# Performance work log

Hardware: AMD Instinct MI355X
Metric: run time of the kernel (lower is better)

The kernel has to match this reference:

```python
import jax, jax.numpy as jnp
import numpy as np

B, MAX_ATOM, F = 512, 256, 256
L_IN, L_OUT = 2, 1


def setup_inputs() -> dict:
    key = jax.random.key(0)
    ks = jax.random.split(key, 8)
    return {
        "node_features": jax.random.normal(ks[0], (B, MAX_ATOM, F), dtype=jnp.float32),
        "inblock_acts": jax.random.normal(ks[1], (L_IN, B, MAX_ATOM, F), dtype=jnp.float32),
        "block_outputs": jax.random.normal(ks[2], (L_OUT, B, MAX_ATOM, F), dtype=jnp.float32),
        "mol_slice": jax.random.randint(ks[3], (B,), 1, MAX_ATOM + 1, dtype=jnp.int32),
        "W_in": jax.random.normal(ks[4], (L_IN, F, F), dtype=jnp.float32) * (1.0 / np.sqrt(F)),
        "W_out": jax.random.normal(ks[5], (L_OUT, F, F), dtype=jnp.float32) * (1.0 / np.sqrt(F)),
        "beta1": jnp.ones((1,), dtype=jnp.float32),
        "beta2": jnp.ones((1,), dtype=jnp.float32),
    }


def reference(node_features, inblock_acts, block_outputs, mol_slice, W_in, W_out, beta1, beta2):
    # Row mask replaces per-graph dynamic slice + zero pad: masked rows stay 0
    # through the row-wise matmuls and through ReLU(0)=0.
    max_atom = node_features.shape[1]
    mask = (jnp.arange(max_atom)[None, :] < mol_slice[:, None]).astype(node_features.dtype)[:, :, None]  # [B,M,1]
    # multi-residual matmul-accumulate over inblock layers and preceding blocks
    x = node_features
    x = x + beta1[0] * jnp.einsum('lbmf,lfo->bmo', inblock_acts, W_in)
    x = x + beta2[0] * jnp.einsum('pbmf,pfo->bmo', block_outputs, W_out)
    return jax.nn.relu(x * mask)  # [B, max_atom, F]
```

## Files before the change

### kernel.cpp

```cpp
#include <hip/hip_runtime.h>
#include <hip/hip_bf16.h>


#define BATCH  512
#define MAXA   256
#define FDIM   256
#define KTOT   768
#define ROWS   131072
#define TILE_M 128
#define BK     64
#define KPAD   72

typedef __attribute__((ext_vector_type(8))) short  short8;
typedef __attribute__((ext_vector_type(4))) float  fx4;

__device__ __forceinline__ unsigned short f2bf(float x) {
  unsigned int u = __builtin_bit_cast(unsigned int, x);
  u += 0x7fffu + ((u >> 16) & 1u);
  return (unsigned short)(u >> 16);
}

__device__ __forceinline__ short8 cvt8(fx4 a, fx4 b) {
  short8 r;
  r[0] = (short)f2bf(a[0]); r[1] = (short)f2bf(a[1]);
  r[2] = (short)f2bf(a[2]); r[3] = (short)f2bf(a[3]);
  r[4] = (short)f2bf(b[0]); r[5] = (short)f2bf(b[1]);
  r[6] = (short)f2bf(b[2]); r[7] = (short)f2bf(b[3]);
  return r;
}

__global__ void prep_weights(const float* __restrict__ Win,
                             const float* __restrict__ Wout,
                             const float* __restrict__ b1,
                             const float* __restrict__ b2,
                             unsigned short* __restrict__ Wt) {
  int id = blockIdx.x * 256 + threadIdx.x;
  int n = id / KTOT;
  int k = id - n * KTOT;
  float beta, w;
  if (k < 512) { beta = b1[0]; w = Win[k * FDIM + n]; }
  else         { beta = b2[0]; w = Wout[(k - 512) * FDIM + n]; }
  Wt[id] = f2bf(beta * w);
}

__launch_bounds__(512, 4)
__global__ void fused_main(const float* __restrict__ node,
                           const float* __restrict__ acts,
                           const float* __restrict__ bouts,
                           const int*   __restrict__ mol_slice,
                           const unsigned short* __restrict__ Wt,
                           float* __restrict__ out) {
  const int tile  = blockIdx.x;
  const int bmol  = tile >> 1;
  const int m0    = (tile & 1) << 7;
  const int slice = mol_slice[bmol];
  const int t     = threadIdx.x;
  const long rowBase = (long)tile * TILE_M;

  if (slice <= m0) {
    fx4 z = {0.f, 0.f, 0.f, 0.f};
    fx4* o4 = (fx4*)(out + rowBase * FDIM);
#pragma unroll
    for (int i = 0; i < 16; ++i) o4[i * 512 + t] = z;
    return;
  }

  __shared__ unsigned short Xs[TILE_M][KPAD];
  __shared__ unsigned short Ws[FDIM][KPAD];

  const int lane = t & 63;
  const int wv   = t >> 6;
  const int wm   = (wv >> 2) << 6;
  const int wn   = (wv & 3) << 6;

  fx4 acc[4][4];
#pragma unroll
  for (int i = 0; i < 4; ++i)
#pragma unroll
    for (int j = 0; j < 4; ++j) acc[i][j] = (fx4){0.f, 0.f, 0.f, 0.f};

  const int xrow = t >> 2;
  const int xc   = (t & 3) << 4;
  const bool xact = (m0 + xrow) < slice;
  const int wrow = t >> 1;
  const int wc   = (t & 1) << 5;

  for (int kk = 0; kk < KTOT; kk += BK) {
    const float* src = (kk < 256) ? acts : ((kk < 512) ? (acts + 33554432) : bouts);
    const int klocal = kk & 255;

    if (xact) {
      const fx4* g = (const fx4*)(src + (rowBase + xrow) * FDIM + klocal + xc);
      fx4 v0 = g[0], v1 = g[1], v2 = g[2], v3 = g[3];
      *(short8*)&Xs[xrow][xc]     = cvt8(v0, v1);
      *(short8*)&Xs[xrow][xc + 8] = cvt8(v2, v3);
    }
    {
      const int4* g = (const int4*)(Wt + (size_t)wrow * KTOT + kk + wc);
      int4 q0 = g[0], q1 = g[1], q2 = g[2], q3 = g[3];
      *(int4*)&Ws[wrow][wc]      = q0;
      *(int4*)&Ws[wrow][wc + 8]  = q1;
      *(int4*)&Ws[wrow][wc + 16] = q2;
      *(int4*)&Ws[wrow][wc + 24] = q3;
    }
    __syncthreads();

#pragma unroll
    for (int s = 0; s < 2; ++s) {
      const int ko = (s << 5) + ((lane >> 4) << 3);
      short8 af[4], bfr[4];
#pragma unroll
      for (int i = 0; i < 4; ++i)
        af[i] = *(const short8*)&Xs[wm + (i << 4) + (lane & 15)][ko];
#pragma unroll
      for (int j = 0; j < 4; ++j)
        bfr[j] = *(const short8*)&Ws[wn + (j << 4) + (lane & 15)][ko];
#pragma unroll
      for (int i = 0; i < 4; ++i)
#pragma unroll
        for (int j = 0; j < 4; ++j)
          acc[i][j] = __builtin_amdgcn_mfma_f32_16x16x32_bf16(af[i], bfr[j], acc[i][j], 0, 0, 0);
    }
    __syncthreads();
  }

  const int cq = lane >> 4;
  const int cl = lane & 15;
#pragma unroll
  for (int i = 0; i < 4; ++i) {
    const int rb = wm + (i << 4) + (cq << 2);
#pragma unroll
    for (int r = 0; r < 4; ++r) {
      const int lrow = rb + r;
      const int m = m0 + lrow;
      const long gro = (rowBase + lrow) * FDIM;
      const bool act = m < slice;
#pragma unroll
      for (int j = 0; j < 4; ++j) {
        const int col = wn + (j << 4) + cl;
        float v = 0.f;
        if (act) {
          v = node[gro + col] + acc[i][j][r];
          v = fmaxf(v, 0.f);
        }
        out[gro + col] = v;
      }
    }
  }
}

extern "C" void kernel_launch(void* const* d_in, const int* in_sizes, int n_in,
                              void* d_out, int out_size, void* d_ws, size_t ws_size,
                              hipStream_t stream) {
  const float* node  = (const float*)d_in[0];
  const float* acts  = (const float*)d_in[1];
  const float* bouts = (const float*)d_in[2];
  const int*   mslc  = (const int*)d_in[3];
  const float* Win   = (const float*)d_in[4];
  const float* Wout  = (const float*)d_in[5];
  const float* b1    = (const float*)d_in[6];
  const float* b2    = (const float*)d_in[7];
  float* out = (float*)d_out;
  unsigned short* Wt = (unsigned short*)d_ws;

  prep_weights<<<dim3(768), dim3(256), 0, stream>>>(Win, Wout, b1, b2, Wt);
  fused_main<<<dim3(1024), dim3(512), 0, stream>>>(node, acts, bouts, mslc, Wt, out);
}
```

Baseline: 571.7 us.

## Swizzle LDS tiles, async-load weights to LDS, prefetch next activation tile

Weights are pre-swizzled into per-K-tile blocks so they can be copied straight into LDS with global_load_lds, bypassing registers. The activation tile for the next K step is loaded into registers while the current step computes. The padded LDS layout is replaced by an XOR swizzle to avoid bank conflicts. Waves whose rows are all past the molecule length skip loads and MFMA work. Explicit waitcnt and barrier handling adds risk of races or ordering mistakes.

```diff
diff --git a/kernel.cpp b/kernel.cpp
--- a/kernel.cpp
+++ b/kernel.cpp
@@ -6,13 +6,14 @@
 #define MAXA   256
 #define FDIM   256
 #define KTOT   768
-#define ROWS   131072
 #define TILE_M 128
 #define BK     64
-#define KPAD   72
+#define NKT    12
 
 typedef __attribute__((ext_vector_type(8))) short  short8;
 typedef __attribute__((ext_vector_type(4))) float  fx4;
+typedef const __attribute__((address_space(1))) unsigned int GASU;
+typedef __attribute__((address_space(3))) unsigned int LASU;
 
 __device__ __forceinline__ unsigned short f2bf(float x) {
   unsigned int u = __builtin_bit_cast(unsigned int, x);
@@ -40,7 +41,10 @@
   float beta, w;
   if (k < 512) { beta = b1[0]; w = Win[k * FDIM + n]; }
   else         { beta = b2[0]; w = Wout[(k - 512) * FDIM + n]; }
-  Wt[id] = f2bf(beta * w);
+  int tt = k >> 6;
+  int kl = k & 63;
+  int dst = (tt << 14) + (((n << 6) | kl) ^ ((n & 7) << 3));
+  Wt[dst] = f2bf(beta * w);
 }
 
 __launch_bounds__(512, 4)
@@ -65,8 +69,8 @@
     return;
   }
 
-  __shared__ unsigned short Xs[TILE_M][KPAD];
-  __shared__ unsigned short Ws[FDIM][KPAD];
+  __shared__ unsigned short Xs[TILE_M * BK];
+  __shared__ unsigned short Ws[FDIM * BK];
 
   const int lane = t & 63;
   const int wv   = t >> 6;
@@ -81,47 +85,74 @@
 
   const int xrow = t >> 2;
   const int xc   = (t & 3) << 4;
-  const bool xact = (m0 + xrow) < slice;
-  const int wrow = t >> 1;
-  const int wc   = (t & 1) << 5;
+  const bool waveX = (m0 + (wv << 4)) < slice;
+  const bool waveC = (m0 + wm) < slice;
+  const long xgbase = (rowBase + xrow) * FDIM + xc;
+  const float* acts2 = acts + 33554432;
 
-  for (int kk = 0; kk < KTOT; kk += BK) {
-    const float* src = (kk < 256) ? acts : ((kk < 512) ? (acts + 33554432) : bouts);
-    const int klocal = kk & 255;
+  fx4 v0, v1, v2, v3;
+  if (waveX) {
+    const fx4* g = (const fx4*)(acts + xgbase);
+    v0 = g[0]; v1 = g[1]; v2 = g[2]; v3 = g[3];
+  }
 
-    if (xact) {
-      const fx4* g = (const fx4*)(src + (rowBase + xrow) * FDIM + klocal + xc);
-      fx4 v0 = g[0], v1 = g[1], v2 = g[2], v3 = g[3];
-      *(short8*)&Xs[xrow][xc]     = cvt8(v0, v1);
-      *(short8*)&Xs[xrow][xc + 8] = cvt8(v2, v3);
+  const char* WtB = (const char*)Wt;
+  char* lW = (char*)Ws + (wv << 10);
+
+  for (int kt = 0; kt < NKT; ++kt) {
+    {
+      const char* gW = WtB + (kt << 15) + (wv << 10) + (lane << 4);
+#pragma unroll
+      for (int r = 0; r < 4; ++r)
+        __builtin_amdgcn_global_load_lds((GASU*)(const void*)(gW + (r << 13)),
+                                         (LASU*)(void*)(lW + (r << 13)), 16, 0, 0);
     }
-    {
-      const int4* g = (const int4*)(Wt + (size_t)wrow * KTOT + kk + wc);
-      int4 q0 = g[0], q1 = g[1], q2 = g[2], q3 = g[3];
-      *(int4*)&Ws[wrow][wc]      = q0;
-      *(int4*)&Ws[wrow][wc + 8]  = q1;
-      *(int4*)&Ws[wrow][wc + 16] = q2;
-      *(int4*)&Ws[wrow][wc + 24] = q3;
+
+    if (waveX) {
+      asm volatile("s_waitcnt vmcnt(4)" ::: "memory");
+      short8 pa = cvt8(v0, v1);
+      short8 pb = cvt8(v2, v3);
+      const int ba = ((xrow << 7) + (xc << 1)) ^ ((xrow & 7) << 4);
+      *(short8*)((char*)Xs + ba)        = pa;
+      *(short8*)((char*)Xs + (ba ^ 16)) = pb;
     }
-    __syncthreads();
 
+    const bool pre = waveX && (kt != NKT - 1);
+    if (pre) {
+      const int kkn = (kt + 1) << 6;
+      const float* srcn = (kkn < 256) ? acts : ((kkn < 512) ? acts2 : bouts);
+      const fx4* g = (const fx4*)(srcn + xgbase + (kkn & 255));
+      v0 = g[0]; v1 = g[1]; v2 = g[2]; v3 = g[3];
+    }
+
+    if (pre) asm volatile("s_waitcnt vmcnt(4)" ::: "memory");
+    else     asm volatile("s_waitcnt vmcnt(0)" ::: "memory");
+    asm volatile("s_waitcnt lgkmcnt(0)" ::: "memory");
+    __builtin_amdgcn_s_barrier();
+
+    if (waveC) {
 #pragma unroll
-    for (int s = 0; s < 2; ++s) {
-      const int ko = (s << 5) + ((lane >> 4) << 3);
-      short8 af[4], bfr[4];
+      for (int s = 0; s < 2; ++s) {
+        const int ko2 = ((s << 5) + ((lane >> 4) << 3)) << 1;
+        short8 af[4], bfr[4];
 #pragma unroll
-      for (int i = 0; i < 4; ++i)
-        af[i] = *(const short8*)&Xs[wm + (i << 4) + (lane & 15)][ko];
+        for (int i = 0; i < 4; ++i) {
+          const int m = wm + (i << 4) + (lane & 15);
+          af[i] = *(const short8*)((const char*)Xs + (((m << 7) + ko2) ^ ((m & 7) << 4)));
+        }
 #pragma unroll
-      for (int j = 0; j < 4; ++j)
-        bfr[j] = *(const short8*)&Ws[wn + (j << 4) + (lane & 15)][ko];
+        for (int j = 0; j < 4; ++j) {
+          const int n = wn + (j << 4) + (lane & 15);
+          bfr[j] = *(const short8*)((const char*)Ws + (((n << 7) + ko2) ^ ((n & 7) << 4)));
+        }
 #pragma unroll
-      for (int i = 0; i < 4; ++i)
+        for (int i = 0; i < 4; ++i)
 #pragma unroll
-        for (int j = 0; j < 4; ++j)
-          acc[i][j] = __builtin_amdgcn_mfma_f32_16x16x32_bf16(af[i], bfr[j], acc[i][j], 0, 0, 0);
+          for (int j = 0; j < 4; ++j)
+            acc[i][j] = __builtin_amdgcn_mfma_f32_16x16x32_bf16(af[i], bfr[j], acc[i][j], 0, 0, 0);
+      }
     }
-    __syncthreads();
+    __builtin_amdgcn_s_barrier();
   }
 
   const int cq = lane >> 4;
```

After: 578.2 us. About the same (+1.1%).

## Drop LDS staging and load MFMA fragments directly from global with 64-row tiles

Applied to the files above, without the earlier changes.

Removes the shared-memory tiles and both barriers per K step. Each wave now reads its fp32 activation fragments and bf16 weight fragments straight from global memory, converting the activations in registers before the MFMAs. The row tile shrinks from 128 to 64, so there are twice as many 256-thread blocks and more fully masked tiles take the early zero-fill exit. In exchange, all four waves of a block reload the same activation rows through the cache, and rows past the molecule length inside an active tile are no longer skipped on load.

```diff
diff --git a/kernel.cpp b/kernel.cpp
--- a/kernel.cpp
+++ b/kernel.cpp
@@ -6,10 +6,8 @@
 #define MAXA   256
 #define FDIM   256
 #define KTOT   768
-#define ROWS   131072
-#define TILE_M 128
-#define BK     64
-#define KPAD   72
+#define TILE_M 64
+#define NTILES 2048
 
 typedef __attribute__((ext_vector_type(8))) short  short8;
 typedef __attribute__((ext_vector_type(4))) float  fx4;
@@ -43,7 +41,7 @@
   Wt[id] = f2bf(beta * w);
 }
 
-__launch_bounds__(512, 4)
+__launch_bounds__(256, 3)
 __global__ void fused_main(const float* __restrict__ node,
                            const float* __restrict__ acts,
                            const float* __restrict__ bouts,
@@ -51,8 +49,8 @@
                            const unsigned short* __restrict__ Wt,
                            float* __restrict__ out) {
   const int tile  = blockIdx.x;
-  const int bmol  = tile >> 1;
-  const int m0    = (tile & 1) << 7;
+  const int bmol  = tile >> 2;
+  const int m0    = (tile & 3) << 6;
   const int slice = mol_slice[bmol];
   const int t     = threadIdx.x;
   const long rowBase = (long)tile * TILE_M;
@@ -61,17 +59,15 @@
     fx4 z = {0.f, 0.f, 0.f, 0.f};
     fx4* o4 = (fx4*)(out + rowBase * FDIM);
 #pragma unroll
-    for (int i = 0; i < 16; ++i) o4[i * 512 + t] = z;
+    for (int i = 0; i < 16; ++i) o4[i * 256 + t] = z;
     return;
   }
 
-  __shared__ unsigned short Xs[TILE_M][KPAD];
-  __shared__ unsigned short Ws[FDIM][KPAD];
-
   const int lane = t & 63;
   const int wv   = t >> 6;
-  const int wm   = (wv >> 2) << 6;
-  const int wn   = (wv & 3) << 6;
+  const int wn   = wv << 6;
+  const int r15  = lane & 15;
+  const int kl   = (lane >> 4) << 3;
 
   fx4 acc[4][4];
 #pragma unroll
@@ -79,56 +75,54 @@
 #pragma unroll
     for (int j = 0; j < 4; ++j) acc[i][j] = (fx4){0.f, 0.f, 0.f, 0.f};
 
-  const int xrow = t >> 2;
-  const int xc   = (t & 3) << 4;
-  const bool xact = (m0 + xrow) < slice;
-  const int wrow = t >> 1;
-  const int wc   = (t & 1) << 5;
+  long aoff[4];
+#pragma unroll
+  for (int i = 0; i < 4; ++i)
+    aoff[i] = (rowBase + (i << 4) + r15) * (long)FDIM + kl;
+  const unsigned short* wb[4];
+#pragma unroll
+  for (int j = 0; j < 4; ++j)
+    wb[j] = Wt + (wn + (j << 4) + r15) * KTOT + kl;
 
-  for (int kk = 0; kk < KTOT; kk += BK) {
-    const float* src = (kk < 256) ? acts : ((kk < 512) ? (acts + 33554432) : bouts);
-    const int klocal = kk & 255;
-
-    if (xact) {
-      const fx4* g = (const fx4*)(src + (rowBase + xrow) * FDIM + klocal + xc);
-      fx4 v0 = g[0], v1 = g[1], v2 = g[2], v3 = g[3];
-      *(short8*)&Xs[xrow][xc]     = cvt8(v0, v1);
-      *(short8*)&Xs[xrow][xc + 8] = cvt8(v2, v3);
-    }
-    {
-      const int4* g = (const int4*)(Wt + (size_t)wrow * KTOT + kk + wc);
-      int4 q0 = g[0], q1 = g[1], q2 = g[2], q3 = g[3];
-      *(int4*)&Ws[wrow][wc]      = q0;
-      *(int4*)&Ws[wrow][wc + 8]  = q1;
-      *(int4*)&Ws[wrow][wc + 16] = q2;
-      *(int4*)&Ws[wrow][wc + 24] = q3;
-    }
-    __syncthreads();
+  const float* acts2 = acts + 33554432;
 
 #pragma unroll
-    for (int s = 0; s < 2; ++s) {
-      const int ko = (s << 5) + ((lane >> 4) << 3);
-      short8 af[4], bfr[4];
+  for (int seg = 0; seg < 3; ++seg) {
+    const float* src = (seg == 0) ? acts : ((seg == 1) ? acts2 : bouts);
+    const int segk = seg << 8;
+    for (int t4 = 0; t4 < 4; ++t4) {
+      const int k0 = t4 << 6;
 #pragma unroll
-      for (int i = 0; i < 4; ++i)
-        af[i] = *(const short8*)&Xs[wm + (i << 4) + (lane & 15)][ko];
-#pragma unroll
-      for (int j = 0; j < 4; ++j)
-        bfr[j] = *(const short8*)&Ws[wn + (j << 4) + (lane & 15)][ko];
-#pragma unroll
-      for (int i = 0; i < 4; ++i)
+      for (int s = 0; s < 2; ++s) {
+        const int ks = k0 + (s << 5);
+        short8 bfr[4];
 #pragma unroll
         for (int j = 0; j < 4; ++j)
-          acc[i][j] = __builtin_amdgcn_mfma_f32_16x16x32_bf16(af[i], bfr[j], acc[i][j], 0, 0, 0);
+          bfr[j] = *(const short8*)(wb[j] + segk + ks);
+        fx4 u0[4], u1[4];
+#pragma unroll
+        for (int i = 0; i < 4; ++i) {
+          const float* p = src + aoff[i] + ks;
+          u0[i] = *(const fx4*)p;
+          u1[i] = *(const fx4*)(p + 4);
+        }
+        short8 af[4];
+#pragma unroll
+        for (int i = 0; i < 4; ++i) af[i] = cvt8(u0[i], u1[i]);
+#pragma unroll
+        for (int i = 0; i < 4; ++i)
+#pragma unroll
+          for (int j = 0; j < 4; ++j)
+            acc[i][j] = __builtin_amdgcn_mfma_f32_16x16x32_bf16(af[i], bfr[j], acc[i][j], 0, 0, 0);
+      }
     }
-    __syncthreads();
   }
 
   const int cq = lane >> 4;
   const int cl = lane & 15;
 #pragma unroll
   for (int i = 0; i < 4; ++i) {
-    const int rb = wm + (i << 4) + (cq << 2);
+    const int rb = (i << 4) + (cq << 2);
 #pragma unroll
     for (int r = 0; r < 4; ++r) {
       const int lrow = rb + r;
@@ -164,5 +158,5 @@
   unsigned short* Wt = (unsigned short*)d_ws;
 
   prep_weights<<<dim3(768), dim3(256), 0, stream>>>(Win, Wout, b1, b2, Wt);
-  fused_main<<<dim3(1024), dim3(512), 0, stream>>>(node, acts, bouts, mslc, Wt, out);
+  fused_main<<<dim3(NTILES), dim3(256), 0, stream>>>(node, acts, bouts, mslc, Wt, out);
 }
```

After: 761.9 us. 1.33x slower.
